# Optimization experiments

Hardware: AMD Instinct MI355X
Metric: run time of the kernel (lower is better)

## Reference

```python
import jax, jax.numpy as jnp
import numpy as np

N_NODES = 2000
LN_EPS = 1e-5
NEG_SLOPE = 0.2  # PyG GATConv default


def _gat(xg, W, b, a_src, a_dst, src, dst):
    # xg: [G, N, Fin]; single-head GATConv, add_self_loops=False
    h = xg @ W                      # [G, N, H]
    es = h @ a_src                  # [G, N]
    ed = h @ a_dst                  # [G, N]
    e = jax.nn.leaky_relu(es[:, src] + ed[:, dst], NEG_SLOPE)  # [G, E]

    def seg_softmax(e_g):
        m = jax.ops.segment_max(e_g, dst, num_segments=N_NODES)
        ex = jnp.exp(e_g - m[dst])
        s = jax.ops.segment_sum(ex, dst, num_segments=N_NODES)
        return ex / (s[dst] + 1e-16)

    alpha = jax.vmap(seg_softmax)(e)            # [G, E]
    msg = alpha[..., None] * h[:, src]          # [G, E, H]
    agg = jax.vmap(lambda m_: jax.ops.segment_sum(m_, dst, num_segments=N_NODES))(msg)
    return agg + b                              # [G, N, H]


def _gcn_layer(x, W, b, a_src, a_dst, src, dst):
    # x: [B, N, T, F] -- faithfully replicate original permute + raw reshape
    B, N, T, F = x.shape
    x_in = jnp.transpose(x, (0, 2, 1, 3)).reshape(B * T, N, F)
    out = _gat(x_in, W, b, a_src, a_dst, src, dst)          # [B*T, N, H]
    out = jax.nn.gelu(out.reshape(B, T, N, -1), approximate=False)
    # original does .reshape(B, N, T, -1) on a [B,T,N,H]-contiguous tensor
    return out.reshape(B, N, T, -1)


def _lstm(x, Wih, Whh, bih, bhh):
    # x: [BN, T, Fin]; torch LSTM gate order i,f,g,o
    BN, T, _ = x.shape
    H = Whh.shape[1]
    xz = x @ Wih.T + (bih + bhh)                # [BN, T, 4H]

    def step(carry, z_t):
        h, c = carry
        z = z_t + h @ Whh.T
        i, f, g, o = jnp.split(z, 4, axis=-1)
        c = jax.nn.sigmoid(f) * c + jax.nn.sigmoid(i) * jnp.tanh(g)
        h = jax.nn.sigmoid(o) * jnp.tanh(c)
        return (h, c), h

    init = (jnp.zeros((BN, H), x.dtype), jnp.zeros((BN, H), x.dtype))
    _, hs = jax.lax.scan(step, init, jnp.swapaxes(xz, 0, 1))
    return jnp.swapaxes(hs, 0, 1)               # [BN, T, H]


def setup_inputs() -> dict:
    key = jax.random.key(0)
    ks = jax.random.split(key, 20)
    B, N, T, NX, H, PL, NY, E = 2, N_NODES, 24, 8, 64, 12, 1, 32000
    p = {}
    p["x"] = jax.random.normal(ks[0], (B, N, T, NX), jnp.float32)
    p["edge_src"] = jax.random.randint(ks[1], (E,), 0, N, jnp.int32)
    p["edge_dst"] = jax.random.randint(ks[2], (E,), 0, N, jnp.int32)
    p["fc_W"] = jax.random.normal(ks[3], (NX, H), jnp.float32) / np.sqrt(NX)
    p["fc_b"] = jnp.zeros((H,), jnp.float32)
    for i, tag in enumerate(["g1", "g2"]):
        p[f"{tag}_W"] = jax.random.normal(ks[4 + 4 * i], (H, H), jnp.float32) / np.sqrt(H)
        p[f"{tag}_b"] = jnp.zeros((H,), jnp.float32)
        p[f"{tag}_asrc"] = jax.random.normal(ks[5 + 4 * i], (H,), jnp.float32) / np.sqrt(H)
        p[f"{tag}_adst"] = jax.random.normal(ks[6 + 4 * i], (H,), jnp.float32) / np.sqrt(H)
    p["lstm_Wih"] = jax.random.normal(ks[12], (4 * H, H), jnp.float32) / np.sqrt(H)
    p["lstm_Whh"] = jax.random.normal(ks[13], (4 * H, H), jnp.float32) / np.sqrt(H)
    p["lstm_bih"] = jnp.zeros((4 * H,), jnp.float32)
    p["lstm_bhh"] = jnp.zeros((4 * H,), jnp.float32)
    p["ln_g"] = jnp.ones((H,), jnp.float32)
    p["ln_b"] = jnp.zeros((H,), jnp.float32)
    p["dense_W"] = jax.random.normal(ks[14], (H, PL * NY), jnp.float32) / np.sqrt(H)
    p["dense_b"] = jnp.zeros((PL * NY,), jnp.float32)
    return p


def reference(x, edge_src, edge_dst, fc_W, fc_b,
              g1_W, g1_b, g1_asrc, g1_adst,
              g2_W, g2_b, g2_asrc, g2_adst,
              lstm_Wih, lstm_Whh, lstm_bih, lstm_bhh,
              ln_g, ln_b, dense_W, dense_b):
    B, N, T, _ = x.shape
    PRED_LEN, NY = 12, 1
    x_h = x @ fc_W + fc_b                                        # [B,N,T,H]
    g1 = _gcn_layer(x_h, g1_W, g1_b, g1_asrc, g1_adst, edge_src, edge_dst)
    g2 = _gcn_layer(g1, g2_W, g2_b, g2_asrc, g2_adst, edge_src, edge_dst)
    H = g2.shape[-1]
    lout = _lstm(g2.reshape(B * N, T, -1), lstm_Wih, lstm_Whh, lstm_bih, lstm_bhh)
    lout = lout.reshape(B, N, T, H)
    mu = jnp.mean(lout, axis=-1, keepdims=True)
    var = jnp.mean(jnp.square(lout - mu), axis=-1, keepdims=True)
    h = (lout - mu) / jnp.sqrt(var + LN_EPS) * ln_g + ln_b
    out = h[:, :, -1:, :] @ dense_W + dense_b                    # [B,N,1,PL*NY]
    return out.reshape(B, N, PRED_LEN, NY)
```

## Files before the change

### kernel.cpp

```cpp
#include <hip/hip_runtime.h>
#include <hip/hip_bf16.h>
#include <math.h>

#define B_   2
#define N_   2000
#define T_   24
#define NX_  8
#define H_   64
#define G_   (B_*T_)
#define E_   32000
#define BN_  (B_*N_)
#define TH_  (T_*H_)
#define NTH_ (N_*T_*H_)
#define GNH_ (G_*N_*H_)
#define NPARAM_ 43340
#define NPARAM_PAD_ 43392
#define XSTRIDE 1568
#define HPAD 96
#define DEGCAP 64

using bf16 = __hip_bfloat16;
typedef short bf16x8 __attribute__((ext_vector_type(8)));
typedef float f32x4  __attribute__((ext_vector_type(4)));

__device__ __forceinline__ float uasf(unsigned u){ return __uint_as_float(u); }
__device__ __forceinline__ float wave_sum(float v){
  #pragma unroll
  for (int o = 32; o > 0; o >>= 1) v += __shfl_xor(v, o, 64);
  return v;
}
__device__ __forceinline__ float fastrcp(float x){ return __builtin_amdgcn_rcpf(x); }
__device__ __forceinline__ float sigf(float x){ return fastrcp(1.f + __expf(-x)); }
__device__ __forceinline__ float tanhfast(float x){ return 1.f - 2.f*fastrcp(1.f + __expf(2.f*x)); }
__device__ __forceinline__ float gelu_fast(float x){
  float s = x*0.70710678118654752f;
  float a = fabsf(s);
  float t = fastrcp(1.f + 0.3275911f*a);
  float p = t*(0.254829592f + t*(-0.284496736f + t*(1.421413741f + t*(-1.453152027f + t*1.061405429f))));
  float er = 1.f - p*__expf(-a*a);
  er = (s < 0.f) ? -er : er;
  return 0.5f*x*(1.f + er);
}
__device__ __forceinline__ unsigned f2bf_rtn(float f){
  unsigned u = __float_as_uint(f);
  u += 0x7fffu + ((u >> 16) & 1u);
  return u >> 16;
}
__device__ __forceinline__ bf16x8 pack8(float4 a, float4 b){
  bf16x8 v;
  v[0]=(short)f2bf_rtn(a.x); v[1]=(short)f2bf_rtn(a.y);
  v[2]=(short)f2bf_rtn(a.z); v[3]=(short)f2bf_rtn(a.w);
  v[4]=(short)f2bf_rtn(b.x); v[5]=(short)f2bf_rtn(b.y);
  v[6]=(short)f2bf_rtn(b.z); v[7]=(short)f2bf_rtn(b.w);
  return v;
}

struct ConvArgs {
  const void* src[18];
  int off[19];
};
__global__ __launch_bounds__(256) void prep_kernel(
    ConvArgs a, const unsigned* __restrict__ xw,
    float* __restrict__ dst, int* __restrict__ flag,
    int* __restrict__ cnt_g,
    float* __restrict__ wc, float* __restrict__ bc){
  __shared__ int scnt;
  int tid = threadIdx.x;
  if (tid == 0) scnt = 0;
  __syncthreads();
  int c = 0;
  for (int i = tid; i < 4096; i += 256){
    unsigned e = (xw[i] >> 7) & 0xffu;
    if (e >= 100u && e <= 140u) c++;
  }
  atomicAdd(&scnt, c);
  __syncthreads();
  int isbf = (scnt > 3276) ? 1 : 0;
  int bid = blockIdx.x;

  if (bid < 170){
    if (bid == 0 && tid == 0) *flag = isbf;
    int i = bid*256 + tid;
    if (i < NPARAM_){
      int seg = 0;
      while (i >= a.off[seg+1]) seg++;
      int j = i - a.off[seg];
      float v;
      if (isbf) v = uasf(((unsigned)((const unsigned short*)a.src[seg])[j]) << 16);
      else      v = ((const float*)a.src[seg])[j];
      dst[i] = v;
    }
  } else if (bid == 170){
    for (int i = tid; i < N_; i += 256) cnt_g[i] = 0;
  } else {
    int lane = tid & 63, wave = tid >> 6;
    int b = bid - 171;
    const unsigned short* fcWu = (const unsigned short*)a.src[0];
    const unsigned short* fcbu = (const unsigned short*)a.src[1];
    const unsigned short* g1Wu = (const unsigned short*)a.src[2];
    const float* fcWf = (const float*)a.src[0];
    const float* fcbf = (const float*)a.src[1];
    const float* g1Wf = (const float*)a.src[2];
    #pragma unroll
    for (int s = 0; s < 16; ++s){
      int o = b*64 + wave*16 + s;
      int r = o >> 6;
      int n = o & 63;
      float fa, fb;
      if (isbf){
        fa = (r < 8) ? uasf(((unsigned)fcWu[r*64 + lane]) << 16)
                     : uasf(((unsigned)fcbu[lane]) << 16);
        fb = uasf(((unsigned)g1Wu[lane*64 + n]) << 16);
      } else {
        fa = (r < 8) ? fcWf[r*64 + lane] : fcbf[lane];
        fb = g1Wf[lane*64 + n];
      }
      float sv = wave_sum(fa * fb);
      if (lane == 0){
        if (r < 8) wc[r*64 + n] = sv;
        else       bc[n] = sv;
      }
    }
  }
}

__global__ __launch_bounds__(256) void gat_h1_fused_kernel(
    const void* __restrict__ xraw, const int* __restrict__ flag,
    const int* __restrict__ esrc, const int* __restrict__ edst,
    int* __restrict__ cnt_g, int* __restrict__ slot,
    const float* __restrict__ wc, const float* __restrict__ bc,
    const float* __restrict__ asrc, const float* __restrict__ adst,
    unsigned short* __restrict__ hbuf, float* __restrict__ es, float* __restrict__ ed){
  if (blockIdx.x < 125){
    int e = blockIdx.x*256 + threadIdx.x;
    int d = edst[e];
    int pos = atomicAdd(&cnt_g[d], 1);
    if (pos < DEGCAP) slot[(d << 6) + pos] = esrc[e];
  }
  int lane = threadIdx.x & 63, wave = threadIdx.x >> 6;
  int q = lane >> 4, c = lane & 15;
  int isbf = *flag;
  bf16x8 Bf[4];
  #pragma unroll
  for (int nt = 0; nt < 4; ++nt){
    bf16x8 v;
    #pragma unroll
    for (int j = 0; j < 8; ++j)
      v[j] = (q == 0) ? (short)f2bf_rtn(wc[j*64 + nt*16 + c]) : (short)0;
    Bf[nt] = v;
  }
  float bcv[4];
  #pragma unroll
  for (int nt = 0; nt < 4; ++nt) bcv[nt] = bc[nt*16 + c];
  float aS[4], aD[4];
  #pragma unroll
  for (int nt = 0; nt < 4; ++nt){ aS[nt] = asrc[nt*16+c]; aD[nt] = adst[nt*16+c]; }

  int w = blockIdx.x*4 + wave;
  #pragma unroll
  for (int it = 0; it < 2; ++it){
    int tile = w*2 + it;
    int p0 = tile*16;
    int g  = p0 / N_, n0 = p0 - g*N_;
    int bb = g / T_,  tt = g - bb*T_;
    bf16x8 A0;
    #pragma unroll
    for (int j = 0; j < 8; ++j) A0[j] = 0;
    if (q == 0){
      size_t rowelt = ((size_t)(bb*N_ + n0 + c)*T_ + tt)*NX_;
      if (isbf){
        A0 = *(const bf16x8*)((const unsigned short*)xraw + rowelt);
      } else {
        const float4* xr4 = (const float4*)((const float*)xraw + rowelt);
        A0 = pack8(xr4[0], xr4[1]);
      }
    }
    f32x4 acc[4];
    #pragma unroll
    for (int nt = 0; nt < 4; ++nt){ acc[nt][0]=bcv[nt]; acc[nt][1]=bcv[nt]; acc[nt][2]=bcv[nt]; acc[nt][3]=bcv[nt]; }
    #pragma unroll
    for (int nt = 0; nt < 4; ++nt) acc[nt] = __builtin_amdgcn_mfma_f32_16x16x32_bf16(A0, Bf[nt], acc[nt], 0, 0, 0);

    #pragma unroll
    for (int nt = 0; nt < 4; ++nt){
      #pragma unroll
      for (int r = 0; r < 4; ++r)
        hbuf[(size_t)(p0 + q*4 + r)*H_ + nt*16 + c] = (unsigned short)f2bf_rtn(acc[nt][r]);
    }
    #pragma unroll
    for (int r = 0; r < 4; ++r){
      float e1 = acc[0][r]*aS[0] + acc[1][r]*aS[1] + acc[2][r]*aS[2] + acc[3][r]*aS[3];
      float e2 = acc[0][r]*aD[0] + acc[1][r]*aD[1] + acc[2][r]*aD[2] + acc[3][r]*aD[3];
      #pragma unroll
      for (int o = 8; o > 0; o >>= 1){
        e1 += __shfl_xor(e1, o, 64);
        e2 += __shfl_xor(e2, o, 64);
      }
      if (c == 0){
        es[p0 + q*4 + r] = e1;
        ed[p0 + q*4 + r] = e2;
      }
    }
  }
}

__global__ __launch_bounds__(256) void gat_h2_mfma_kernel(
    const unsigned short* __restrict__ xinb, const float* __restrict__ W,
    const float* __restrict__ asrc, const float* __restrict__ adst,
    unsigned short* __restrict__ hbuf, float* __restrict__ es, float* __restrict__ ed){
  int lane = threadIdx.x & 63, wave = threadIdx.x >> 6;
  int q = lane >> 4, c = lane & 15;
  bf16x8 Bf[4][2];
  #pragma unroll
  for (int nt = 0; nt < 4; ++nt){
    #pragma unroll
    for (int ks = 0; ks < 2; ++ks){
      bf16x8 v;
      #pragma unroll
      for (int j = 0; j < 8; ++j)
        v[j] = (short)f2bf_rtn(W[(ks*32 + q*8 + j)*H_ + nt*16 + c]);
      Bf[nt][ks] = v;
    }
  }
  float aS[4], aD[4];
  #pragma unroll
  for (int nt = 0; nt < 4; ++nt){ aS[nt] = asrc[nt*16+c]; aD[nt] = adst[nt*16+c]; }

  int w = blockIdx.x*4 + wave;
  #pragma unroll
  for (int it = 0; it < 2; ++it){
    int tile = w*2 + it;
    int p0 = tile*16;
    int p  = p0 + c;
    int g = p / N_, n = p - g*N_;
    int bb = g / T_, t = g - bb*T_;
    const unsigned short* xr = xinb + (size_t)bb*NTH_ + (size_t)n*TH_ + (size_t)t*H_;
    bf16x8 A0 = *(const bf16x8*)(xr + q*8);
    bf16x8 A1 = *(const bf16x8*)(xr + 32 + q*8);

    f32x4 acc[4];
    #pragma unroll
    for (int nt = 0; nt < 4; ++nt){ acc[nt][0]=0.f; acc[nt][1]=0.f; acc[nt][2]=0.f; acc[nt][3]=0.f; }
    #pragma unroll
    for (int nt = 0; nt < 4; ++nt) acc[nt] = __builtin_amdgcn_mfma_f32_16x16x32_bf16(A0, Bf[nt][0], acc[nt], 0, 0, 0);
    #pragma unroll
    for (int nt = 0; nt < 4; ++nt) acc[nt] = __builtin_amdgcn_mfma_f32_16x16x32_bf16(A1, Bf[nt][1], acc[nt], 0, 0, 0);

    #pragma unroll
    for (int nt = 0; nt < 4; ++nt){
      #pragma unroll
      for (int r = 0; r < 4; ++r)
        hbuf[(size_t)(p0 + q*4 + r)*H_ + nt*16 + c] = (unsigned short)f2bf_rtn(acc[nt][r]);
    }
    #pragma unroll
    for (int r = 0; r < 4; ++r){
      float e1 = acc[0][r]*aS[0] + acc[1][r]*aS[1] + acc[2][r]*aS[2] + acc[3][r]*aS[3];
      float e2 = acc[0][r]*aD[0] + acc[1][r]*aD[1] + acc[2][r]*aD[2] + acc[3][r]*aD[3];
      #pragma unroll
      for (int o = 8; o > 0; o >>= 1){
        e1 += __shfl_xor(e1, o, 64);
        e2 += __shfl_xor(e2, o, 64);
      }
      if (c == 0){
        es[p0 + q*4 + r] = e1;
        ed[p0 + q*4 + r] = e2;
      }
    }
  }
}

__global__ __launch_bounds__(256) void gat_agg_kernel(
    const unsigned short* __restrict__ hbuf, const float* __restrict__ es, const float* __restrict__ ed,
    const int* __restrict__ cnt_g, const int* __restrict__ slot,
    const float* __restrict__ bias, unsigned short* __restrict__ goutb){
  int lane = threadIdx.x & 63, wave = threadIdx.x >> 6;
  int qd = lane >> 4, ln = lane & 15;
  int gd = (blockIdx.x*4 + wave)*4 + qd;
  int g = gd / N_, d = gd - g*N_;
  int start = d << 6;
  int deg = min(cnt_g[d], DEGCAP);
  const float* esg = es + (size_t)g*N_;
  float edv = ed[(size_t)g*N_ + d];
  const char* hg = (const char*)(hbuf + (size_t)g*N_*H_);
  unsigned lanoff = ((unsigned)ln) << 3;
  int hbase = qd << 4;
  int dm = deg;
  dm = max(dm, __shfl_xor(dm, 16, 64));
  dm = max(dm, __shfl_xor(dm, 32, 64));
  int NC = (dm + 15) >> 4;

  int svk[4];
  #pragma unroll
  for (int k = 0; k < 4; ++k) svk[k] = 0;
  #pragma unroll
  for (int k = 0; k < 4; ++k){
    int i = k*16 + ln;
    if (k < NC && i < deg) svk[k] = slot[start + i];
  }
  float exk[4]; float ssum = 0.f;
  #pragma unroll
  for (int k = 0; k < 4; ++k){
    int i = k*16 + ln;
    float e = 0.f;
    if (k < NC && i < deg){
      float v = esg[svk[k]] + edv;
      v = v > 0.f ? v : 0.2f*v;
      e = __expf(fminf(v, 60.f));
    }
    exk[k] = e; ssum += e;
  }
  #pragma unroll
  for (int o = 8; o > 0; o >>= 1) ssum += __shfl_xor(ssum, o, 64);
  float inv = fastrcp(ssum + 1e-16f);
  unsigned pwk[4];
  #pragma unroll
  for (int k = 0; k < 4; ++k)
    pwk[k] = (f2bf_rtn(exk[k]*inv) << 16) | (unsigned)svk[k];

  float a0 = 0.f, a1 = 0.f, a2 = 0.f, a3 = 0.f;
  for (int k = 0; k < NC; ++k){
    unsigned pw = pwk[k];
    int myrem = deg - k*16;
    int remw = dm - k*16; if (remw > 16) remw = 16;
    for (int j0 = 0; j0 < remw; j0 += 8){
      unsigned wv[8]; float aa[8]; unsigned off[8];
      #pragma unroll
      for (int u = 0; u < 8; ++u){
        int j = j0 + u;
        wv[u] = (unsigned)__shfl((int)pw, hbase + j, 64);
        aa[u] = (j < myrem) ? uasf(wv[u] & 0xffff0000u) : 0.f;
        off[u] = ((wv[u] & 0xffffu) << 7) + lanoff;
      }
      uint2 hv[8];
      #pragma unroll
      for (int u = 0; u < 8; ++u)
        hv[u] = *(const uint2*)(hg + off[u]);
      #pragma unroll
      for (int u = 0; u < 8; ++u){
        a0 = fmaf(aa[u], uasf(hv[u].x << 16), a0);
        a1 = fmaf(aa[u], uasf(hv[u].x & 0xffff0000u), a1);
        a2 = fmaf(aa[u], uasf(hv[u].y << 16), a2);
        a3 = fmaf(aa[u], uasf(hv[u].y & 0xffff0000u), a3);
      }
    }
  }
  float4 bv = ((const float4*)bias)[ln];
  uint2 ov;
  ov.x = f2bf_rtn(gelu_fast(a0 + bv.x)) | (f2bf_rtn(gelu_fast(a1 + bv.y)) << 16);
  ov.y = f2bf_rtn(gelu_fast(a2 + bv.z)) | (f2bf_rtn(gelu_fast(a3 + bv.w)) << 16);
  ((uint2*)(goutb + (size_t)gd*H_))[ln] = ov;
}

__global__ __launch_bounds__(256) void lstm_final_kernel(
    const unsigned short* __restrict__ xinb,
    const float* __restrict__ Wih,
    const float* __restrict__ Whh,
    const float* __restrict__ bih, const float* __restrict__ bhh,
    const float* __restrict__ lng, const float* __restrict__ lnb,
    const float* __restrict__ dW, const float* __restrict__ db,
    const int* __restrict__ flag, void* __restrict__ outv){
  __shared__ __align__(16) unsigned short Xlds[4*XSTRIDE];
  __shared__ __align__(16) unsigned short Hlds[2][4*HPAD];
  __shared__ float smH[4][68];
  int tid = threadIdx.x;
  int lane = tid & 63, wave = tid >> 6;
  int q = lane >> 4, c = lane & 15;
  int cc = c >> 2;
  int s0 = blockIdx.x * 4;

  {
    const unsigned short* xg = xinb + (size_t)s0 * TH_;
    #pragma unroll
    for (int ch0 = 0; ch0 < 12; ch0 += 4){
      int ch = ch0 + wave;
      int r = ch / 3, jj = ch - r*3;
      bf16x8 v = *(const bf16x8*)(xg + r*1536 + jj*512 + lane*8);
      *(bf16x8*)(Xlds + r*XSTRIDE + jj*512 + lane*8) = v;
    }
  }

  bf16x8 Bf[4][4];
  #pragma unroll
  for (int g = 0; g < 4; ++g){
    int n = g*64 + wave*16 + c;
    #pragma unroll
    for (int ks = 0; ks < 4; ++ks){
      const float* srcp = (ks < 2) ? (Whh + (size_t)n*64 + ks*32 + q*8)
                                   : (Wih + (size_t)n*64 + (ks-2)*32 + q*8);
      float4 a = ((const float4*)srcp)[0];
      float4 b = ((const float4*)srcp)[1];
      Bf[g][ks] = pack8(a, b);
    }
  }
  float bsum[4];
  #pragma unroll
  for (int g = 0; g < 4; ++g){
    int n = g*64 + wave*16 + c;
    bsum[g] = bih[n] + bhh[n];
  }
  for (int i = tid; i < 4*HPAD; i += 256) Hlds[0][i] = 0;
  float cst = 0.f;
  __syncthreads();

  const unsigned short* xrow = Xlds + cc*XSTRIDE;
  bf16x8 Ax0 = *(const bf16x8*)(xrow + q*8);
  bf16x8 Ax1 = *(const bf16x8*)(xrow + 32 + q*8);

  int buf = 0;
  for (int t = 0; t < T_; ++t){
    bf16x8 Ah0 = *(const bf16x8*)(Hlds[buf] + cc*HPAD + q*8);
    bf16x8 Ah1 = *(const bf16x8*)(Hlds[buf] + cc*HPAD + 32 + q*8);

    f32x4 acc[4];
    #pragma unroll
    for (int g = 0; g < 4; ++g){ acc[g][0]=bsum[g]; acc[g][1]=bsum[g]; acc[g][2]=bsum[g]; acc[g][3]=bsum[g]; }
    #pragma unroll
    for (int g = 0; g < 4; ++g) acc[g] = __builtin_amdgcn_mfma_f32_16x16x32_bf16(Ax0, Bf[g][2], acc[g], 0, 0, 0);
    #pragma unroll
    for (int g = 0; g < 4; ++g) acc[g] = __builtin_amdgcn_mfma_f32_16x16x32_bf16(Ax1, Bf[g][3], acc[g], 0, 0, 0);
    #pragma unroll
    for (int g = 0; g < 4; ++g) acc[g] = __builtin_amdgcn_mfma_f32_16x16x32_bf16(Ah0, Bf[g][0], acc[g], 0, 0, 0);
    #pragma unroll
    for (int g = 0; g < 4; ++g) acc[g] = __builtin_amdgcn_mfma_f32_16x16x32_bf16(Ah1, Bf[g][1], acc[g], 0, 0, 0);

    int tn = (t < T_-1) ? t+1 : T_-1;
    bf16x8 AxN0 = *(const bf16x8*)(xrow + tn*64 + q*8);
    bf16x8 AxN1 = *(const bf16x8*)(xrow + tn*64 + 32 + q*8);

    float zi = acc[0][0], zf = acc[1][0], zg = acc[2][0], zo = acc[3][0];
    cst = sigf(zf)*cst + sigf(zi)*tanhfast(zg);
    float hv = sigf(zo)*tanhfast(cst);

    if (t == T_-1){
      smH[q][wave*16 + c] = hv;
    } else {
      Hlds[buf^1][q*HPAD + wave*16 + c] = (unsigned short)f2bf_rtn(hv);
      __syncthreads();
      buf ^= 1;
    }
    Ax0 = AxN0; Ax1 = AxN1;
  }
  __syncthreads();

  int isbf = *flag;
  {
    int s = wave;
    float h = smH[s][lane];
    float mu = wave_sum(h) * (1.f/64.f);
    float dev = h - mu;
    float var = wave_sum(dev*dev) * (1.f/64.f);
    float hn = dev * rsqrtf(var + 1e-5f) * lng[lane] + lnb[lane];
    smH[s][lane] = hn;
    if (lane < 12){
      float o = db[lane];
      #pragma unroll
      for (int k = 0; k < 64; ++k) o = fmaf(smH[s][k], dW[k*12 + lane], o);
      size_t oi = (size_t)(s0 + s)*12 + lane;
      if (isbf) ((unsigned short*)outv)[oi] = (unsigned short)f2bf_rtn(o);
      else      ((float*)outv)[oi] = o;
    }
  }
}

extern "C" void kernel_launch(void* const* d_in, const int* in_sizes, int n_in,
                              void* d_out, int out_size, void* d_ws, size_t ws_size,
                              hipStream_t stream) {
  const int* esrc = (const int*)d_in[1];
  const int* edst = (const int*)d_in[2];

  static const int sizes[18] = {512, 64, 4096, 64, 64, 64, 4096, 64, 64, 64,
                                16384, 16384, 256, 256, 64, 64, 768, 12};
  static const int srcidx[18] = {3, 4, 5, 6, 7, 8, 9, 10, 11, 12,
                                 13, 14, 15, 16, 17, 18, 19, 20};
  ConvArgs ca;
  {
    int acc = 0;
    for (int i = 0; i < 18; ++i){ ca.src[i] = d_in[srcidx[i]]; ca.off[i] = acc; acc += sizes[i]; }
    ca.off[18] = acc;
  }

  float* P     = (float*)d_ws;
  float* bufA  = P + NPARAM_PAD_;
  float* bufB  = bufA + (size_t)GNH_/2 + 64;
  float* esb   = bufB + (size_t)GNH_/2 + 64;
  float* edb   = esb  + (size_t)G_*N_;
  int*   cnt_g = (int*)(edb + (size_t)G_*N_);
  int*   slot  = cnt_g + N_;
  int*   flag  = slot + N_*DEGCAP;
  float* wcb   = (float*)(flag + 1);
  unsigned short* goutb = (unsigned short*)bufA;
  unsigned short* hbuf  = (unsigned short*)bufB;

  const float* pg1b = P + 4672;
  const float* pg1as= P + 4736;
  const float* pg1ad= P + 4800;
  const float* pg2W = P + 4864;
  const float* pg2b = P + 8960;
  const float* pg2as= P + 9024;
  const float* pg2ad= P + 9088;
  const float* pWih = P + 9152;
  const float* pWhh = P + 25536;
  const float* pbih = P + 41920;
  const float* pbhh = P + 42176;
  const float* plng = P + 42432;
  const float* plnb = P + 42496;
  const float* pdW  = P + 42560;
  const float* pdb  = P + 43328;

  prep_kernel<<<180, 256, 0, stream>>>(ca, (const unsigned*)d_in[0],
                                       P, flag, cnt_g, wcb, wcb + 512);

  gat_h1_fused_kernel<<<750, 256, 0, stream>>>(d_in[0], flag, esrc, edst, cnt_g, slot,
                                               wcb, wcb + 512, pg1as, pg1ad, hbuf, esb, edb);
  gat_agg_kernel<<<6000, 256, 0, stream>>>(hbuf, esb, edb, cnt_g, slot, pg1b, goutb);

  gat_h2_mfma_kernel<<<750, 256, 0, stream>>>(goutb, pg2W, pg2as, pg2ad, hbuf, esb, edb);
  gat_agg_kernel<<<6000, 256, 0, stream>>>(hbuf, esb, edb, cnt_g, slot, pg2b, goutb);

  lstm_final_kernel<<<1000, 256, 0, stream>>>(goutb, pWih, pWhh, pbih, pbhh,
                                              plng, plnb, pdW, pdb, flag, d_out);
}
```

Before: 216.0 us.

## Restructure LSTM kernel to one wave per sequence with precomputed input projections

The LSTM kernel changes from 4 waves sharing 4 sequences (with per-step LDS round trips and block barriers) to one 64-thread block per sequence. The input projection for all 24 timesteps is computed up front with MFMA into an LDS buffer. The recurrence then runs only the Whh MFMAs and passes the hidden state between lanes with shuffles, so no barriers are needed inside the loop. The trade-offs are 16 MFMA tiles of which only one row is used per step (wasted matrix work), 4000 small blocks, and 24KB of LDS per block, which may limit occupancy.

```diff
diff --git a/kernel.cpp b/kernel.cpp
--- a/kernel.cpp
+++ b/kernel.cpp
@@ -15,8 +15,6 @@
 #define GNH_ (G_*N_*H_)
 #define NPARAM_ 43340
 #define NPARAM_PAD_ 43392
-#define XSTRIDE 1568
-#define HPAD 96
 #define DEGCAP 64
 
 using bf16 = __hip_bfloat16;
@@ -351,7 +349,7 @@
   ((uint2*)(goutb + (size_t)gd*H_))[ln] = ov;
 }
 
-__global__ __launch_bounds__(256) void lstm_final_kernel(
+__global__ __launch_bounds__(64) void lstm_final_kernel(
     const unsigned short* __restrict__ xinb,
     const float* __restrict__ Wih,
     const float* __restrict__ Whh,
@@ -359,106 +357,120 @@
     const float* __restrict__ lng, const float* __restrict__ lnb,
     const float* __restrict__ dW, const float* __restrict__ db,
     const int* __restrict__ flag, void* __restrict__ outv){
-  __shared__ __align__(16) unsigned short Xlds[4*XSTRIDE];
-  __shared__ __align__(16) unsigned short Hlds[2][4*HPAD];
-  __shared__ float smH[4][68];
-  int tid = threadIdx.x;
-  int lane = tid & 63, wave = tid >> 6;
+  __shared__ __align__(16) float zbuf[T_*256];
+  int lane = threadIdx.x;
   int q = lane >> 4, c = lane & 15;
-  int cc = c >> 2;
-  int s0 = blockIdx.x * 4;
-
-  {
-    const unsigned short* xg = xinb + (size_t)s0 * TH_;
-    #pragma unroll
-    for (int ch0 = 0; ch0 < 12; ch0 += 4){
-      int ch = ch0 + wave;
-      int r = ch / 3, jj = ch - r*3;
-      bf16x8 v = *(const bf16x8*)(xg + r*1536 + jj*512 + lane*8);
-      *(bf16x8*)(Xlds + r*XSTRIDE + jj*512 + lane*8) = v;
-    }
-  }
-
-  bf16x8 Bf[4][4];
-  #pragma unroll
-  for (int g = 0; g < 4; ++g){
-    int n = g*64 + wave*16 + c;
-    #pragma unroll
-    for (int ks = 0; ks < 4; ++ks){
-      const float* srcp = (ks < 2) ? (Whh + (size_t)n*64 + ks*32 + q*8)
-                                   : (Wih + (size_t)n*64 + (ks-2)*32 + q*8);
-      float4 a = ((const float4*)srcp)[0];
-      float4 b = ((const float4*)srcp)[1];
-      Bf[g][ks] = pack8(a, b);
-    }
-  }
-  float bsum[4];
-  #pragma unroll
-  for (int g = 0; g < 4; ++g){
-    int n = g*64 + wave*16 + c;
-    bsum[g] = bih[n] + bhh[n];
-  }
-  for (int i = tid; i < 4*HPAD; i += 256) Hlds[0][i] = 0;
-  float cst = 0.f;
+  int seq = blockIdx.x;
+  int isbf = *flag;
+
+  float bsv[16];
+  #pragma unroll
+  for (int nt = 0; nt < 16; ++nt){ int n = nt*16 + c; bsv[nt] = bih[n] + bhh[n]; }
+
+  bf16x8 Bf[16][2];
+  #pragma unroll
+  for (int nt = 0; nt < 16; ++nt){
+    int n = nt*16 + c;
+    #pragma unroll
+    for (int ks = 0; ks < 2; ++ks){
+      const float* p = Wih + (size_t)n*64 + ks*32 + q*8;
+      Bf[nt][ks] = pack8(((const float4*)p)[0], ((const float4*)p)[1]);
+    }
+  }
+
+  const unsigned short* xs = xinb + (size_t)seq*TH_;
+  #pragma unroll
+  for (int tile = 0; tile < 2; ++tile){
+    int t_ = tile*16 + c;
+    bf16x8 Ax0, Ax1;
+    if (t_ < T_){
+      const unsigned short* xr = xs + (size_t)t_*64;
+      Ax0 = *(const bf16x8*)(xr + q*8);
+      Ax1 = *(const bf16x8*)(xr + 32 + q*8);
+    } else {
+      #pragma unroll
+      for (int j = 0; j < 8; ++j){ Ax0[j] = 0; Ax1[j] = 0; }
+    }
+    f32x4 acc[16];
+    #pragma unroll
+    for (int nt = 0; nt < 16; ++nt){ acc[nt][0]=bsv[nt]; acc[nt][1]=bsv[nt]; acc[nt][2]=bsv[nt]; acc[nt][3]=bsv[nt]; }
+    #pragma unroll
+    for (int nt = 0; nt < 16; ++nt) acc[nt] = __builtin_amdgcn_mfma_f32_16x16x32_bf16(Ax0, Bf[nt][0], acc[nt], 0, 0, 0);
+    #pragma unroll
+    for (int nt = 0; nt < 16; ++nt) acc[nt] = __builtin_amdgcn_mfma_f32_16x16x32_bf16(Ax1, Bf[nt][1], acc[nt], 0, 0, 0);
+    #pragma unroll
+    for (int r = 0; r < 4; ++r){
+      int t = tile*16 + q*4 + r;
+      if (t < T_){
+        #pragma unroll
+        for (int m = 0; m < 4; ++m){
+          f32x4 wv;
+          wv[0] = acc[m][r]; wv[1] = acc[m+4][r]; wv[2] = acc[m+8][r]; wv[3] = acc[m+12][r];
+          *(f32x4*)(zbuf + t*256 + (m*16 + c)*4) = wv;
+        }
+      }
+    }
+  }
+
+  #pragma unroll
+  for (int nt = 0; nt < 16; ++nt){
+    int n = nt*16 + c;
+    #pragma unroll
+    for (int ks = 0; ks < 2; ++ks){
+      const float* p = Whh + (size_t)n*64 + ks*32 + q*8;
+      Bf[nt][ks] = pack8(((const float4*)p)[0], ((const float4*)p)[1]);
+    }
+  }
   __syncthreads();
 
-  const unsigned short* xrow = Xlds + cc*XSTRIDE;
-  bf16x8 Ax0 = *(const bf16x8*)(xrow + q*8);
-  bf16x8 Ax1 = *(const bf16x8*)(xrow + 32 + q*8);
-
-  int buf = 0;
+  bf16x8 Ah0, Ah1;
+  #pragma unroll
+  for (int j = 0; j < 8; ++j){ Ah0[j] = 0; Ah1[j] = 0; }
+  float cst = 0.f, hv = 0.f;
+  int sbase = q*8;
+
   for (int t = 0; t < T_; ++t){
-    bf16x8 Ah0 = *(const bf16x8*)(Hlds[buf] + cc*HPAD + q*8);
-    bf16x8 Ah1 = *(const bf16x8*)(Hlds[buf] + cc*HPAD + 32 + q*8);
-
-    f32x4 acc[4];
-    #pragma unroll
-    for (int g = 0; g < 4; ++g){ acc[g][0]=bsum[g]; acc[g][1]=bsum[g]; acc[g][2]=bsum[g]; acc[g][3]=bsum[g]; }
-    #pragma unroll
-    for (int g = 0; g < 4; ++g) acc[g] = __builtin_amdgcn_mfma_f32_16x16x32_bf16(Ax0, Bf[g][2], acc[g], 0, 0, 0);
-    #pragma unroll
-    for (int g = 0; g < 4; ++g) acc[g] = __builtin_amdgcn_mfma_f32_16x16x32_bf16(Ax1, Bf[g][3], acc[g], 0, 0, 0);
-    #pragma unroll
-    for (int g = 0; g < 4; ++g) acc[g] = __builtin_amdgcn_mfma_f32_16x16x32_bf16(Ah0, Bf[g][0], acc[g], 0, 0, 0);
-    #pragma unroll
-    for (int g = 0; g < 4; ++g) acc[g] = __builtin_amdgcn_mfma_f32_16x16x32_bf16(Ah1, Bf[g][1], acc[g], 0, 0, 0);
-
-    int tn = (t < T_-1) ? t+1 : T_-1;
-    bf16x8 AxN0 = *(const bf16x8*)(xrow + tn*64 + q*8);
-    bf16x8 AxN1 = *(const bf16x8*)(xrow + tn*64 + 32 + q*8);
-
-    float zi = acc[0][0], zf = acc[1][0], zg = acc[2][0], zo = acc[3][0];
-    cst = sigf(zf)*cst + sigf(zi)*tanhfast(zg);
-    float hv = sigf(zo)*tanhfast(cst);
-
-    if (t == T_-1){
-      smH[q][wave*16 + c] = hv;
-    } else {
-      Hlds[buf^1][q*HPAD + wave*16 + c] = (unsigned short)f2bf_rtn(hv);
-      __syncthreads();
-      buf ^= 1;
-    }
-    Ax0 = AxN0; Ax1 = AxN1;
-  }
+    f32x4 zv = *(const f32x4*)(zbuf + t*256 + lane*4);
+
+    f32x4 acc[16];
+    #pragma unroll
+    for (int nt = 0; nt < 16; ++nt){ acc[nt][0]=0.f; acc[nt][1]=0.f; acc[nt][2]=0.f; acc[nt][3]=0.f; }
+    #pragma unroll
+    for (int nt = 0; nt < 16; ++nt) acc[nt] = __builtin_amdgcn_mfma_f32_16x16x32_bf16(Ah0, Bf[nt][0], acc[nt], 0, 0, 0);
+    #pragma unroll
+    for (int nt = 0; nt < 16; ++nt) acc[nt] = __builtin_amdgcn_mfma_f32_16x16x32_bf16(Ah1, Bf[nt][1], acc[nt], 0, 0, 0);
+
+    float ag[4];
+    #pragma unroll
+    for (int g = 0; g < 4; ++g){
+      float a01 = (q & 1) ? acc[4*g+1][0] : acc[4*g+0][0];
+      float a23 = (q & 1) ? acc[4*g+3][0] : acc[4*g+2][0];
+      ag[g] = ((q & 2) ? a23 : a01) + zv[g];
+    }
+    cst = sigf(ag[1])*cst + sigf(ag[0])*tanhfast(ag[2]);
+    hv = sigf(ag[3])*tanhfast(cst);
+
+    int pkb = (int)f2bf_rtn(hv);
+    #pragma unroll
+    for (int j = 0; j < 8; ++j){
+      Ah0[j] = (short)__shfl(pkb, sbase + j, 64);
+      Ah1[j] = (short)__shfl(pkb, 32 + sbase + j, 64);
+    }
+  }
+
+  float mu = wave_sum(hv) * (1.f/64.f);
+  float dev = hv - mu;
+  float var = wave_sum(dev*dev) * (1.f/64.f);
+  float hn = dev * rsqrtf(var + 1e-5f) * lng[lane] + lnb[lane];
+  zbuf[lane] = hn;
   __syncthreads();
-
-  int isbf = *flag;
-  {
-    int s = wave;
-    float h = smH[s][lane];
-    float mu = wave_sum(h) * (1.f/64.f);
-    float dev = h - mu;
-    float var = wave_sum(dev*dev) * (1.f/64.f);
-    float hn = dev * rsqrtf(var + 1e-5f) * lng[lane] + lnb[lane];
-    smH[s][lane] = hn;
-    if (lane < 12){
-      float o = db[lane];
-      #pragma unroll
-      for (int k = 0; k < 64; ++k) o = fmaf(smH[s][k], dW[k*12 + lane], o);
-      size_t oi = (size_t)(s0 + s)*12 + lane;
-      if (isbf) ((unsigned short*)outv)[oi] = (unsigned short)f2bf_rtn(o);
-      else      ((float*)outv)[oi] = o;
-    }
+  if (lane < 12){
+    float o = db[lane];
+    #pragma unroll
+    for (int k = 0; k < 64; ++k) o = fmaf(zbuf[k], dW[k*12 + lane], o);
+    size_t oi = (size_t)seq*12 + lane;
+    if (isbf) ((unsigned short*)outv)[oi] = (unsigned short)f2bf_rtn(o);
+    else      ((float*)outv)[oi] = o;
   }
 }
 
@@ -517,6 +529,6 @@
   gat_h2_mfma_kernel<<<750, 256, 0, stream>>>(goutb, pg2W, pg2as, pg2ad, hbuf, esb, edb);
   gat_agg_kernel<<<6000, 256, 0, stream>>>(hbuf, esb, edb, cnt_g, slot, pg2b, goutb);
 
-  lstm_final_kernel<<<1000, 256, 0, stream>>>(goutb, pWih, pWhh, pbih, pbhh,
-                                              plng, plnb, pdW, pdb, flag, d_out);
-}
+  lstm_final_kernel<<<BN_, 64, 0, stream>>>(goutb, pWih, pWhh, pbih, pbhh,
+                                            plng, plnb, pdW, pdb, flag, d_out);
+}
```

Result: slower. 306.6 us (+42.0%).

## Fold layer-2 GAT projection into aggregation and precompute attention logits

Applied to the files above, without the earlier changes.

Removes the separate layer-2 linear-projection kernel. The attention scores es2/ed2 are computed in the first aggregation kernel by dotting its GELU output with precomputed W2·a_src and W2·a_dst vectors, which the prep kernel now builds. The second aggregation gathers raw layer-1 outputs (in the permuted [B,N,T,H] layout) and applies W2 via MFMA after aggregation, relying on linearity. This saves one kernel launch and a full hbuf write and read, at the cost of extra MFMA and LDS work inside aggregation and bf16 rounding of the aggregate before the matmul.

```diff
diff --git a/kernel.cpp b/kernel.cpp
--- a/kernel.cpp
+++ b/kernel.cpp
@@ -92,7 +92,7 @@
     }
   } else if (bid == 170){
     for (int i = tid; i < N_; i += 256) cnt_g[i] = 0;
-  } else {
+  } else if (bid < 180){
     int lane = tid & 63, wave = tid >> 6;
     int b = bid - 171;
     const unsigned short* fcWu = (const unsigned short*)a.src[0];
@@ -121,6 +121,22 @@
         else       bc[n] = sv;
       }
     }
+  } else {
+    int lane = tid & 63, wave = tid >> 6;
+    int isA = (bid == 180);
+    const unsigned short* g2Wu = (const unsigned short*)a.src[6];
+    const float* g2Wf = (const float*)a.src[6];
+    const unsigned short* au = (const unsigned short*)a.src[isA ? 8 : 9];
+    const float* af = (const float*)a.src[isA ? 8 : 9];
+    float fb = isbf ? uasf(((unsigned)au[lane]) << 16) : af[lane];
+    #pragma unroll
+    for (int s = 0; s < 16; ++s){
+      int k = wave*16 + s;
+      float fa = isbf ? uasf(((unsigned)g2Wu[k*64 + lane]) << 16)
+                      : uasf(f2bf_rtn(g2Wf[k*64 + lane]) << 16);
+      float sv = wave_sum(fa * fb);
+      if (lane == 0) wc[(isA ? 576 : 640) + k] = sv;
+    }
   }
 }
 
@@ -204,75 +220,12 @@
   }
 }
 
-__global__ __launch_bounds__(256) void gat_h2_mfma_kernel(
-    const unsigned short* __restrict__ xinb, const float* __restrict__ W,
-    const float* __restrict__ asrc, const float* __restrict__ adst,
-    unsigned short* __restrict__ hbuf, float* __restrict__ es, float* __restrict__ ed){
-  int lane = threadIdx.x & 63, wave = threadIdx.x >> 6;
-  int q = lane >> 4, c = lane & 15;
-  bf16x8 Bf[4][2];
-  #pragma unroll
-  for (int nt = 0; nt < 4; ++nt){
-    #pragma unroll
-    for (int ks = 0; ks < 2; ++ks){
-      bf16x8 v;
-      #pragma unroll
-      for (int j = 0; j < 8; ++j)
-        v[j] = (short)f2bf_rtn(W[(ks*32 + q*8 + j)*H_ + nt*16 + c]);
-      Bf[nt][ks] = v;
-    }
-  }
-  float aS[4], aD[4];
-  #pragma unroll
-  for (int nt = 0; nt < 4; ++nt){ aS[nt] = asrc[nt*16+c]; aD[nt] = adst[nt*16+c]; }
-
-  int w = blockIdx.x*4 + wave;
-  #pragma unroll
-  for (int it = 0; it < 2; ++it){
-    int tile = w*2 + it;
-    int p0 = tile*16;
-    int p  = p0 + c;
-    int g = p / N_, n = p - g*N_;
-    int bb = g / T_, t = g - bb*T_;
-    const unsigned short* xr = xinb + (size_t)bb*NTH_ + (size_t)n*TH_ + (size_t)t*H_;
-    bf16x8 A0 = *(const bf16x8*)(xr + q*8);
-    bf16x8 A1 = *(const bf16x8*)(xr + 32 + q*8);
-
-    f32x4 acc[4];
-    #pragma unroll
-    for (int nt = 0; nt < 4; ++nt){ acc[nt][0]=0.f; acc[nt][1]=0.f; acc[nt][2]=0.f; acc[nt][3]=0.f; }
-    #pragma unroll
-    for (int nt = 0; nt < 4; ++nt) acc[nt] = __builtin_amdgcn_mfma_f32_16x16x32_bf16(A0, Bf[nt][0], acc[nt], 0, 0, 0);
-    #pragma unroll
-    for (int nt = 0; nt < 4; ++nt) acc[nt] = __builtin_amdgcn_mfma_f32_16x16x32_bf16(A1, Bf[nt][1], acc[nt], 0, 0, 0);
-
-    #pragma unroll
-    for (int nt = 0; nt < 4; ++nt){
-      #pragma unroll
-      for (int r = 0; r < 4; ++r)
-        hbuf[(size_t)(p0 + q*4 + r)*H_ + nt*16 + c] = (unsigned short)f2bf_rtn(acc[nt][r]);
-    }
-    #pragma unroll
-    for (int r = 0; r < 4; ++r){
-      float e1 = acc[0][r]*aS[0] + acc[1][r]*aS[1] + acc[2][r]*aS[2] + acc[3][r]*aS[3];
-      float e2 = acc[0][r]*aD[0] + acc[1][r]*aD[1] + acc[2][r]*aD[2] + acc[3][r]*aD[3];
-      #pragma unroll
-      for (int o = 8; o > 0; o >>= 1){
-        e1 += __shfl_xor(e1, o, 64);
-        e2 += __shfl_xor(e2, o, 64);
-      }
-      if (c == 0){
-        es[p0 + q*4 + r] = e1;
-        ed[p0 + q*4 + r] = e2;
-      }
-    }
-  }
-}
-
-__global__ __launch_bounds__(256) void gat_agg_kernel(
+__global__ __launch_bounds__(256) void gat_agg1_kernel(
     const unsigned short* __restrict__ hbuf, const float* __restrict__ es, const float* __restrict__ ed,
     const int* __restrict__ cnt_g, const int* __restrict__ slot,
-    const float* __restrict__ bias, unsigned short* __restrict__ goutb){
+    const float* __restrict__ bias, unsigned short* __restrict__ goutb,
+    const float* __restrict__ wa2, const float* __restrict__ wd2,
+    float* __restrict__ es2, float* __restrict__ ed2){
   int lane = threadIdx.x & 63, wave = threadIdx.x >> 6;
   int qd = lane >> 4, ln = lane & 15;
   int gd = (blockIdx.x*4 + wave)*4 + qd;
@@ -345,10 +298,160 @@
     }
   }
   float4 bv = ((const float4*)bias)[ln];
+  float g0 = gelu_fast(a0 + bv.x), g1 = gelu_fast(a1 + bv.y);
+  float g2v = gelu_fast(a2 + bv.z), g3 = gelu_fast(a3 + bv.w);
   uint2 ov;
-  ov.x = f2bf_rtn(gelu_fast(a0 + bv.x)) | (f2bf_rtn(gelu_fast(a1 + bv.y)) << 16);
-  ov.y = f2bf_rtn(gelu_fast(a2 + bv.z)) | (f2bf_rtn(gelu_fast(a3 + bv.w)) << 16);
+  ov.x = f2bf_rtn(g0) | (f2bf_rtn(g1) << 16);
+  ov.y = f2bf_rtn(g2v) | (f2bf_rtn(g3) << 16);
   ((uint2*)(goutb + (size_t)gd*H_))[ln] = ov;
+
+  float h0 = uasf(ov.x << 16), h1v = uasf(ov.x & 0xffff0000u);
+  float h2v = uasf(ov.y << 16), h3v = uasf(ov.y & 0xffff0000u);
+  f32x4 wa = *(const f32x4*)(wa2 + ln*4);
+  f32x4 wd = *(const f32x4*)(wd2 + ln*4);
+  float e1 = h0*wa[0] + h1v*wa[1] + h2v*wa[2] + h3v*wa[3];
+  float e2 = h0*wd[0] + h1v*wd[1] + h2v*wd[2] + h3v*wd[3];
+  #pragma unroll
+  for (int o = 8; o > 0; o >>= 1){
+    e1 += __shfl_xor(e1, o, 64);
+    e2 += __shfl_xor(e2, o, 64);
+  }
+  if (ln == 0){
+    int bbp = gd / (N_*T_);
+    int rem = gd - bbp*(N_*T_);
+    int np  = rem / T_;
+    int tp  = rem - np*T_;
+    int pprime = (bbp*T_ + tp)*N_ + np;
+    es2[pprime] = e1;
+    ed2[pprime] = e2;
+  }
+}
+
+__global__ __launch_bounds__(256) void gat_agg2_kernel(
+    const unsigned short* __restrict__ goutb, const float* __restrict__ es, const float* __restrict__ ed,
+    const int* __restrict__ cnt_g, const int* __restrict__ slot,
+    const float* __restrict__ W, const float* __restrict__ b2,
+    unsigned short* __restrict__ outb){
+  __shared__ __align__(16) float vlds[4*256];
+  int lane = threadIdx.x & 63, wave = threadIdx.x >> 6;
+  int qd = lane >> 4, ln = lane & 15;
+  int gd = (blockIdx.x*4 + wave)*4 + qd;
+  int g = gd / N_, d = gd - g*N_;
+  int bb2 = g / T_, t2 = g - bb2*T_;
+  int start = d << 6;
+  int deg = min(cnt_g[d], DEGCAP);
+  const float* esg = es + (size_t)g*N_;
+  float edv = ed[(size_t)g*N_ + d];
+  const char* hgb = (const char*)goutb + (size_t)bb2*(size_t)(NTH_*2) + (size_t)t2*128 + (((unsigned)ln) << 3);
+  int hbase = qd << 4;
+  int dm = deg;
+  dm = max(dm, __shfl_xor(dm, 16, 64));
+  dm = max(dm, __shfl_xor(dm, 32, 64));
+  int NC = (dm + 15) >> 4;
+
+  bf16x8 Bf[4][2];
+  #pragma unroll
+  for (int nt = 0; nt < 4; ++nt){
+    #pragma unroll
+    for (int ks = 0; ks < 2; ++ks){
+      bf16x8 v;
+      #pragma unroll
+      for (int j = 0; j < 8; ++j)
+        v[j] = (short)f2bf_rtn(W[(ks*32 + qd*8 + j)*H_ + nt*16 + ln]);
+      Bf[nt][ks] = v;
+    }
+  }
+  float bcv[4];
+  #pragma unroll
+  for (int nt = 0; nt < 4; ++nt) bcv[nt] = b2[nt*16 + ln];
+
+  int svk[4];
+  #pragma unroll
+  for (int k = 0; k < 4; ++k) svk[k] = 0;
+  #pragma unroll
+  for (int k = 0; k < 4; ++k){
+    int i = k*16 + ln;
+    if (k < NC && i < deg) svk[k] = slot[start + i];
+  }
+  float exk[4]; float ssum = 0.f;
+  #pragma unroll
+  for (int k = 0; k < 4; ++k){
+    int i = k*16 + ln;
+    float e = 0.f;
+    if (k < NC && i < deg){
+      float v = esg[svk[k]] + edv;
+      v = v > 0.f ? v : 0.2f*v;
+      e = __expf(fminf(v, 60.f));
+    }
+    exk[k] = e; ssum += e;
+  }
+  #pragma unroll
+  for (int o = 8; o > 0; o >>= 1) ssum += __shfl_xor(ssum, o, 64);
+  float inv = fastrcp(ssum + 1e-16f);
+  unsigned pwk[4];
+  #pragma unroll
+  for (int k = 0; k < 4; ++k)
+    pwk[k] = (f2bf_rtn(exk[k]*inv) << 16) | (unsigned)svk[k];
+
+  float a0 = 0.f, a1 = 0.f, a2 = 0.f, a3 = 0.f;
+  for (int k = 0; k < NC; ++k){
+    unsigned pw = pwk[k];
+    int myrem = deg - k*16;
+    int remw = dm - k*16; if (remw > 16) remw = 16;
+    for (int j0 = 0; j0 < remw; j0 += 8){
+      unsigned wv[8]; float aa[8]; unsigned off[8];
+      #pragma unroll
+      for (int u = 0; u < 8; ++u){
+        int j = j0 + u;
+        wv[u] = (unsigned)__shfl((int)pw, hbase + j, 64);
+        aa[u] = (j < myrem) ? uasf(wv[u] & 0xffff0000u) : 0.f;
+        off[u] = (wv[u] & 0xffffu) * 3072u;
+      }
+      uint2 hv[8];
+      #pragma unroll
+      for (int u = 0; u < 8; ++u)
+        hv[u] = *(const uint2*)(hgb + off[u]);
+      #pragma unroll
+      for (int u = 0; u < 8; ++u){
+        a0 = fmaf(aa[u], uasf(hv[u].x << 16), a0);
+        a1 = fmaf(aa[u], uasf(hv[u].x & 0xffff0000u), a1);
+        a2 = fmaf(aa[u], uasf(hv[u].y << 16), a2);
+        a3 = fmaf(aa[u], uasf(hv[u].y & 0xffff0000u), a3);
+      }
+    }
+  }
+
+  unsigned short* vu = (unsigned short*)vlds + wave*512;
+  uint2 vp;
+  vp.x = f2bf_rtn(a0) | (f2bf_rtn(a1) << 16);
+  vp.y = f2bf_rtn(a2) | (f2bf_rtn(a3) << 16);
+  *(uint2*)(vu + qd*64 + ln*4) = vp;
+  bf16x8 Af0 = *(const bf16x8*)(vu + (ln & 3)*64 + qd*8);
+  bf16x8 Af1 = *(const bf16x8*)(vu + (ln & 3)*64 + 32 + qd*8);
+
+  f32x4 acc[4];
+  #pragma unroll
+  for (int nt = 0; nt < 4; ++nt){ acc[nt][0]=0.f; acc[nt][1]=0.f; acc[nt][2]=0.f; acc[nt][3]=0.f; }
+  #pragma unroll
+  for (int nt = 0; nt < 4; ++nt) acc[nt] = __builtin_amdgcn_mfma_f32_16x16x32_bf16(Af0, Bf[nt][0], acc[nt], 0, 0, 0);
+  #pragma unroll
+  for (int nt = 0; nt < 4; ++nt) acc[nt] = __builtin_amdgcn_mfma_f32_16x16x32_bf16(Af1, Bf[nt][1], acc[nt], 0, 0, 0);
+
+  float* vf = vlds + wave*256;
+  if (qd == 0){
+    #pragma unroll
+    for (int nt = 0; nt < 4; ++nt){
+      #pragma unroll
+      for (int r = 0; r < 4; ++r)
+        vf[r*64 + nt*16 + ln] = acc[nt][r] + bcv[nt];
+    }
+  }
+  __syncthreads();
+  f32x4 vo = *(const f32x4*)(vf + qd*64 + ln*4);
+  uint2 ov;
+  ov.x = f2bf_rtn(gelu_fast(vo[0])) | (f2bf_rtn(gelu_fast(vo[1])) << 16);
+  ov.y = f2bf_rtn(gelu_fast(vo[2])) | (f2bf_rtn(gelu_fast(vo[3])) << 16);
+  ((uint2*)(outb + (size_t)gd*H_))[ln] = ov;
 }
 
 __global__ __launch_bounds__(256) void lstm_final_kernel(
@@ -488,6 +591,8 @@
   int*   slot  = cnt_g + N_;
   int*   flag  = slot + N_*DEGCAP;
   float* wcb   = (float*)(flag + 1);
+  float* es2b  = wcb + 704;
+  float* ed2b  = es2b + (size_t)G_*N_;
   unsigned short* goutb = (unsigned short*)bufA;
   unsigned short* hbuf  = (unsigned short*)bufB;
 
@@ -496,8 +601,6 @@
   const float* pg1ad= P + 4800;
   const float* pg2W = P + 4864;
   const float* pg2b = P + 8960;
-  const float* pg2as= P + 9024;
-  const float* pg2ad= P + 9088;
   const float* pWih = P + 9152;
   const float* pWhh = P + 25536;
   const float* pbih = P + 41920;
@@ -507,16 +610,18 @@
   const float* pdW  = P + 42560;
   const float* pdb  = P + 43328;
 
-  prep_kernel<<<180, 256, 0, stream>>>(ca, (const unsigned*)d_in[0],
+  prep_kernel<<<182, 256, 0, stream>>>(ca, (const unsigned*)d_in[0],
                                        P, flag, cnt_g, wcb, wcb + 512);
 
   gat_h1_fused_kernel<<<750, 256, 0, stream>>>(d_in[0], flag, esrc, edst, cnt_g, slot,
                                                wcb, wcb + 512, pg1as, pg1ad, hbuf, esb, edb);
-  gat_agg_kernel<<<6000, 256, 0, stream>>>(hbuf, esb, edb, cnt_g, slot, pg1b, goutb);
-
-  gat_h2_mfma_kernel<<<750, 256, 0, stream>>>(goutb, pg2W, pg2as, pg2ad, hbuf, esb, edb);
-  gat_agg_kernel<<<6000, 256, 0, stream>>>(hbuf, esb, edb, cnt_g, slot, pg2b, goutb);
-
-  lstm_final_kernel<<<1000, 256, 0, stream>>>(goutb, pWih, pWhh, pbih, pbhh,
+
+  gat_agg1_kernel<<<6000, 256, 0, stream>>>(hbuf, esb, edb, cnt_g, slot, pg1b, goutb,
+                                            wcb + 576, wcb + 640, es2b, ed2b);
+
+  gat_agg2_kernel<<<6000, 256, 0, stream>>>(goutb, es2b, ed2b, cnt_g, slot,
+                                            pg2W, pg2b, hbuf);
+
+  lstm_final_kernel<<<1000, 256, 0, stream>>>(hbuf, pWih, pWhh, pbih, pbhh,
                                               plng, plnb, pdW, pdb, flag, d_out);
 }
```

New measurement: 234.2 us. 1.08x slower.
